# Kernel optimization log

Hardware: AMD Instinct MI355X
Metric: run time of the kernel (lower is better)

Reference implementation:

```python
import jax, jax.numpy as jnp
import numpy as np

NUM_KERNELS = 50
KERNEL_DIM = 5


def setup_inputs() -> dict:
    key = jax.random.key(0)
    k1, k2 = jax.random.split(key)
    B, F = 1024, 512
    x = jax.random.normal(k1, (B, F), dtype=jnp.float32)
    # glorot-uniform-ish scale for T
    fan_in, fan_out = F, NUM_KERNELS * KERNEL_DIM
    limit = float(np.sqrt(6.0 / (fan_in + fan_out)))
    T = jax.random.uniform(k2, (F, fan_out), dtype=jnp.float32, minval=-limit, maxval=limit)
    return {"x": x, "T": T}


def reference(x, T):
    B = x.shape[0]
    # M: [B, K, D]
    M = (x @ T).reshape(B, NUM_KERNELS, KERNEL_DIM)
    # pairwise diffs: [B, K, D, B]  (M[i,k,d] - M[j,k,d])
    diffs = M[:, :, :, None] - jnp.transpose(M, (1, 2, 0))[None, :, :, :]
    abs_diffs = jnp.sum(jnp.abs(diffs), axis=2)          # [B, K, B]
    minibatch_features = jnp.sum(jnp.exp(-abs_diffs), axis=2)  # [B, K]
    return jnp.concatenate([x, minibatch_features], axis=1)
```

## Files before the change

### kernel.cpp

```cpp
#include <hip/hip_runtime.h>

#define B_SZ 1024
#define F_SZ 512
#define NK   50
#define KD   5
#define C_SZ 250
#define OUTW 562
#define PLANE (C_SZ * B_SZ)
#define NT   16
#define TILE 64
#define NPAIRS 136
#define PART_ELEMS (NK * NT * B_SZ)
#define LOG2E 1.44269504088896340736f

__global__ __launch_bounds__(256) void gemm_copy_kernel(const float* __restrict__ x,
                                                        const float* __restrict__ T,
                                                        float* __restrict__ ws2,
                                                        float* __restrict__ out,
                                                        int zero_feat) {
    const int t = threadIdx.x;

    if (blockIdx.x >= 256) {
        const int b = blockIdx.x - 256;
#pragma unroll
        for (int r = 0; r < 8; ++r) {
            const int row = b * 8 + r;
            const float2* src = (const float2*)(x + (size_t)row * F_SZ);
            float2* dst = (float2*)(out + (size_t)row * OUTW);
            dst[t] = src[t];
            if (zero_feat && t < NK) out[(size_t)row * OUTW + F_SZ + t] = 0.0f;
        }
        return;
    }

    const int rt = blockIdx.x & 127;
    const int ks = blockIdx.x >> 7;
    if (t >= C_SZ) return;
    const int r0 = rt * 8;
    const int f0 = ks * 256;

    float acc[8] = {0.f, 0.f, 0.f, 0.f, 0.f, 0.f, 0.f, 0.f};
    const float* xp = x + (size_t)r0 * F_SZ + f0;
    const float* Tp = T + (size_t)f0 * C_SZ + t;

#pragma unroll 8
    for (int f = 0; f < 256; ++f) {
        const float tv = Tp[(size_t)f * C_SZ];
#pragma unroll
        for (int r = 0; r < 8; ++r)
            acc[r] += xp[r * F_SZ + f] * tv;
    }

    float* dst = ws2 + ((size_t)(ks * C_SZ + t)) * B_SZ + r0;
    float4 lo = make_float4(acc[0] * LOG2E, acc[1] * LOG2E,
                            acc[2] * LOG2E, acc[3] * LOG2E);
    float4 hi = make_float4(acc[4] * LOG2E, acc[5] * LOG2E,
                            acc[6] * LOG2E, acc[7] * LOG2E);
    ((float4*)dst)[0] = lo;
    ((float4*)dst)[1] = hi;
}

template <bool ATOMIC>
__global__ __launch_bounds__(256) void pair_kernel(const float* __restrict__ ws2,
                                                   float* __restrict__ part,
                                                   float* __restrict__ out) {
    const int bid = blockIdx.x;
    const int k = bid / NPAIRS;
    int p = bid - k * NPAIRS;
    int ti = 0;
    while (p >= NT - ti) { p -= NT - ti; ++ti; }
    const int tj = ti + p;

    const int t    = threadIdx.x;
    const int lane = t & 63;
    const int jq   = t >> 6;

    __shared__ __align__(16) float qi[KD][TILE];
    __shared__ __align__(16) float qj[KD][TILE];
    __shared__ float et[TILE][TILE + 1];
    __shared__ float rowp[4][TILE];
    __shared__ float colp[4][TILE];

    const float* pa = ws2 + (size_t)k * KD * B_SZ;
    const float* pb = pa + (size_t)PLANE;

    if (t < TILE) {
#pragma unroll
        for (int d = 0; d < KD; ++d) {
            const int row = ti * TILE + t;
            qi[d][t] = pa[d * B_SZ + row] + pb[d * B_SZ + row];
        }
    } else if (t < 2 * TILE) {
        const int l = t - TILE;
#pragma unroll
        for (int d = 0; d < KD; ++d) {
            const int row = tj * TILE + l;
            qj[d][l] = pa[d * B_SZ + row] + pb[d * B_SZ + row];
        }
    }
    __syncthreads();

    float m0 = qi[0][lane], m1 = qi[1][lane], m2 = qi[2][lane],
          m3 = qi[3][lane], m4 = qi[4][lane];
    float acc = 0.0f;
#pragma unroll
    for (int c4 = 0; c4 < 4; ++c4) {
        const int j0 = jq * 16 + c4 * 4;
        const float4 c0 = *(const float4*)&qj[0][j0];
        const float4 c1 = *(const float4*)&qj[1][j0];
        const float4 c2 = *(const float4*)&qj[2][j0];
        const float4 c3 = *(const float4*)&qj[3][j0];
        const float4 c4_ = *(const float4*)&qj[4][j0];
#define PAIR_ONE(C, JOFF)                                                        \
        {                                                                        \
            const float s = __builtin_fabsf(m0 - c0.C)                           \
                          + __builtin_fabsf(m1 - c1.C)                           \
                          + __builtin_fabsf(m2 - c2.C)                           \
                          + __builtin_fabsf(m3 - c3.C)                           \
                          + __builtin_fabsf(m4 - c4_.C);                         \
            const float e = __builtin_amdgcn_exp2f(-s);                          \
            acc += e;                                                            \
            et[j0 + JOFF][lane] = e;                                             \
        }
        PAIR_ONE(x, 0) PAIR_ONE(y, 1) PAIR_ONE(z, 2) PAIR_ONE(w, 3)
#undef PAIR_ONE
    }
    rowp[jq][lane] = acc;
    __syncthreads();

    if (ti != tj) {
        float csum = 0.0f;
#pragma unroll
        for (int e = 0; e < 16; ++e) csum += et[lane][jq * 16 + e];
        colp[jq][lane] = csum;
    }

    if (t < TILE) {
        const float r = rowp[0][t] + rowp[1][t] + rowp[2][t] + rowp[3][t];
        const int row = ti * TILE + t;
        if (ATOMIC) atomicAdd(&out[(size_t)row * OUTW + F_SZ + k], r);
        else        part[((size_t)(k * NT + tj)) * B_SZ + row] = r;
    }

    if (ti != tj) {
        __syncthreads();
        if (t < TILE) {
            const float c = colp[0][t] + colp[1][t] + colp[2][t] + colp[3][t];
            const int row = tj * TILE + t;
            if (ATOMIC) atomicAdd(&out[(size_t)row * OUTW + F_SZ + k], c);
            else        part[((size_t)(k * NT + ti)) * B_SZ + row] = c;
        }
    }
}

__global__ __launch_bounds__(256) void reduce_kernel(const float* __restrict__ part,
                                                     float* __restrict__ out) {
    const int k = blockIdx.x >> 2;
    const int i = ((blockIdx.x & 3) << 8) | threadIdx.x;
    float s = 0.0f;
#pragma unroll
    for (int sp = 0; sp < NT; ++sp)
        s += part[((size_t)(k * NT + sp)) * B_SZ + i];
    out[(size_t)i * OUTW + F_SZ + k] = s;
}

extern "C" void kernel_launch(void* const* d_in, const int* in_sizes, int n_in,
                              void* d_out, int out_size, void* d_ws, size_t ws_size,
                              hipStream_t stream) {
    const float* x = (const float*)d_in[0];
    const float* T = (const float*)d_in[1];
    float* out = (float*)d_out;
    float* ws2 = (float*)d_ws;
    float* part = ws2 + 2 * (size_t)PLANE;

    const size_t need = (size_t)(2 * PLANE + PART_ELEMS) * 4;
    const int fast = (ws_size >= need);

    gemm_copy_kernel<<<384, 256, 0, stream>>>(x, T, ws2, out, fast ? 0 : 1);

    if (fast) {
        pair_kernel<false><<<NK * NPAIRS, 256, 0, stream>>>(ws2, part, out);
        reduce_kernel<<<200, 256, 0, stream>>>(part, out);
    } else {
        pair_kernel<true><<<NK * NPAIRS, 256, 0, stream>>>(ws2, nullptr, out);
    }
}
```

Before: 35.70 us.

## Drop GEMM split-K and recompute symmetric pair tile instead of LDS transpose

```diff
diff --git a/kernel.cpp b/kernel.cpp
--- a/kernel.cpp
+++ b/kernel.cpp
@@ -15,13 +15,13 @@
 
 __global__ __launch_bounds__(256) void gemm_copy_kernel(const float* __restrict__ x,
                                                         const float* __restrict__ T,
-                                                        float* __restrict__ ws2,
+                                                        float* __restrict__ mp,
                                                         float* __restrict__ out,
                                                         int zero_feat) {
     const int t = threadIdx.x;
 
-    if (blockIdx.x >= 256) {
-        const int b = blockIdx.x - 256;
+    if (blockIdx.x >= 512) {
+        const int b = blockIdx.x - 512;
 #pragma unroll
         for (int r = 0; r < 8; ++r) {
             const int row = b * 8 + r;
@@ -33,35 +33,27 @@
         return;
     }
 
-    const int rt = blockIdx.x & 127;
-    const int ks = blockIdx.x >> 7;
+    const int rt = blockIdx.x;
     if (t >= C_SZ) return;
-    const int r0 = rt * 8;
-    const int f0 = ks * 256;
+    const int r0 = rt * 2;
 
-    float acc[8] = {0.f, 0.f, 0.f, 0.f, 0.f, 0.f, 0.f, 0.f};
-    const float* xp = x + (size_t)r0 * F_SZ + f0;
-    const float* Tp = T + (size_t)f0 * C_SZ + t;
+    float acc0 = 0.f, acc1 = 0.f;
+    const float* xp = x + (size_t)r0 * F_SZ;
+    const float* Tp = T + t;
 
-#pragma unroll 8
-    for (int f = 0; f < 256; ++f) {
+#pragma unroll 16
+    for (int f = 0; f < F_SZ; ++f) {
         const float tv = Tp[(size_t)f * C_SZ];
-#pragma unroll
-        for (int r = 0; r < 8; ++r)
-            acc[r] += xp[r * F_SZ + f] * tv;
+        acc0 += xp[f] * tv;
+        acc1 += xp[F_SZ + f] * tv;
     }
 
-    float* dst = ws2 + ((size_t)(ks * C_SZ + t)) * B_SZ + r0;
-    float4 lo = make_float4(acc[0] * LOG2E, acc[1] * LOG2E,
-                            acc[2] * LOG2E, acc[3] * LOG2E);
-    float4 hi = make_float4(acc[4] * LOG2E, acc[5] * LOG2E,
-                            acc[6] * LOG2E, acc[7] * LOG2E);
-    ((float4*)dst)[0] = lo;
-    ((float4*)dst)[1] = hi;
+    float2* dst = (float2*)(mp + (size_t)t * B_SZ + r0);
+    *dst = make_float2(acc0 * LOG2E, acc1 * LOG2E);
 }
 
 template <bool ATOMIC>
-__global__ __launch_bounds__(256) void pair_kernel(const float* __restrict__ ws2,
+__global__ __launch_bounds__(256) void pair_kernel(const float* __restrict__ mp,
                                                    float* __restrict__ part,
                                                    float* __restrict__ out) {
     const int bid = blockIdx.x;
@@ -73,83 +65,73 @@
 
     const int t    = threadIdx.x;
     const int lane = t & 63;
-    const int jq   = t >> 6;
+    const int jq   = __builtin_amdgcn_readfirstlane(threadIdx.x >> 6);
 
-    __shared__ __align__(16) float qi[KD][TILE];
-    __shared__ __align__(16) float qj[KD][TILE];
-    __shared__ float et[TILE][TILE + 1];
     __shared__ float rowp[4][TILE];
     __shared__ float colp[4][TILE];
 
-    const float* pa = ws2 + (size_t)k * KD * B_SZ;
-    const float* pb = pa + (size_t)PLANE;
+    const float* pk = mp + (size_t)k * (KD * B_SZ);
+    const int bi = ti * TILE;
+    const int bj = tj * TILE;
 
-    if (t < TILE) {
+    float mi[KD], mj[KD];
 #pragma unroll
-        for (int d = 0; d < KD; ++d) {
-            const int row = ti * TILE + t;
-            qi[d][t] = pa[d * B_SZ + row] + pb[d * B_SZ + row];
-        }
-    } else if (t < 2 * TILE) {
-        const int l = t - TILE;
-#pragma unroll
-        for (int d = 0; d < KD; ++d) {
-            const int row = tj * TILE + l;
-            qj[d][l] = pa[d * B_SZ + row] + pb[d * B_SZ + row];
-        }
+    for (int d = 0; d < KD; ++d) {
+        mi[d] = pk[d * B_SZ + bi + lane];
+        mj[d] = pk[d * B_SZ + bj + lane];
     }
-    __syncthreads();
 
-    float m0 = qi[0][lane], m1 = qi[1][lane], m2 = qi[2][lane],
-          m3 = qi[3][lane], m4 = qi[4][lane];
-    float acc = 0.0f;
+    const bool diag = (ti == tj);
+    float acci = 0.f, accj = 0.f;
+
+#define ESUM(mm, c0v, c1v, c2v, c3v, c4v, C)                                     \
+    __builtin_amdgcn_exp2f(-(__builtin_fabsf(mm[0] - c0v.C)                      \
+                           + __builtin_fabsf(mm[1] - c1v.C)                      \
+                           + __builtin_fabsf(mm[2] - c2v.C)                      \
+                           + __builtin_fabsf(mm[3] - c3v.C)                      \
+                           + __builtin_fabsf(mm[4] - c4v.C)))
+
 #pragma unroll
     for (int c4 = 0; c4 < 4; ++c4) {
         const int j0 = jq * 16 + c4 * 4;
-        const float4 c0 = *(const float4*)&qj[0][j0];
-        const float4 c1 = *(const float4*)&qj[1][j0];
-        const float4 c2 = *(const float4*)&qj[2][j0];
-        const float4 c3 = *(const float4*)&qj[3][j0];
-        const float4 c4_ = *(const float4*)&qj[4][j0];
-#define PAIR_ONE(C, JOFF)                                                        \
-        {                                                                        \
-            const float s = __builtin_fabsf(m0 - c0.C)                           \
-                          + __builtin_fabsf(m1 - c1.C)                           \
-                          + __builtin_fabsf(m2 - c2.C)                           \
-                          + __builtin_fabsf(m3 - c3.C)                           \
-                          + __builtin_fabsf(m4 - c4_.C);                         \
-            const float e = __builtin_amdgcn_exp2f(-s);                          \
-            acc += e;                                                            \
-            et[j0 + JOFF][lane] = e;                                             \
+
+        const float4 cj0 = *(const float4*)(pk + 0 * B_SZ + bj + j0);
+        const float4 cj1 = *(const float4*)(pk + 1 * B_SZ + bj + j0);
+        const float4 cj2 = *(const float4*)(pk + 2 * B_SZ + bj + j0);
+        const float4 cj3 = *(const float4*)(pk + 3 * B_SZ + bj + j0);
+        const float4 cj4 = *(const float4*)(pk + 4 * B_SZ + bj + j0);
+        acci += ESUM(mi, cj0, cj1, cj2, cj3, cj4, x);
+        acci += ESUM(mi, cj0, cj1, cj2, cj3, cj4, y);
+        acci += ESUM(mi, cj0, cj1, cj2, cj3, cj4, z);
+        acci += ESUM(mi, cj0, cj1, cj2, cj3, cj4, w);
+
+        if (!diag) {
+            const float4 ci0 = *(const float4*)(pk + 0 * B_SZ + bi + j0);
+            const float4 ci1 = *(const float4*)(pk + 1 * B_SZ + bi + j0);
+            const float4 ci2 = *(const float4*)(pk + 2 * B_SZ + bi + j0);
+            const float4 ci3 = *(const float4*)(pk + 3 * B_SZ + bi + j0);
+            const float4 ci4 = *(const float4*)(pk + 4 * B_SZ + bi + j0);
+            accj += ESUM(mj, ci0, ci1, ci2, ci3, ci4, x);
+            accj += ESUM(mj, ci0, ci1, ci2, ci3, ci4, y);
+            accj += ESUM(mj, ci0, ci1, ci2, ci3, ci4, z);
+            accj += ESUM(mj, ci0, ci1, ci2, ci3, ci4, w);
         }
-        PAIR_ONE(x, 0) PAIR_ONE(y, 1) PAIR_ONE(z, 2) PAIR_ONE(w, 3)
-#undef PAIR_ONE
     }
-    rowp[jq][lane] = acc;
+#undef ESUM
+
+    rowp[jq][lane] = acci;
+    if (!diag) colp[jq][lane] = accj;
     __syncthreads();
-
-    if (ti != tj) {
-        float csum = 0.0f;
-#pragma unroll
-        for (int e = 0; e < 16; ++e) csum += et[lane][jq * 16 + e];
-        colp[jq][lane] = csum;
-    }
 
     if (t < TILE) {
         const float r = rowp[0][t] + rowp[1][t] + rowp[2][t] + rowp[3][t];
-        const int row = ti * TILE + t;
-        if (ATOMIC) atomicAdd(&out[(size_t)row * OUTW + F_SZ + k], r);
-        else        part[((size_t)(k * NT + tj)) * B_SZ + row] = r;
-    }
-
-    if (ti != tj) {
-        __syncthreads();
-        if (t < TILE) {
-            const float c = colp[0][t] + colp[1][t] + colp[2][t] + colp[3][t];
-            const int row = tj * TILE + t;
-            if (ATOMIC) atomicAdd(&out[(size_t)row * OUTW + F_SZ + k], c);
-            else        part[((size_t)(k * NT + ti)) * B_SZ + row] = c;
-        }
+        if (ATOMIC) atomicAdd(&out[(size_t)(bi + t) * OUTW + F_SZ + k], r);
+        else        part[(size_t)(k * NT + tj) * B_SZ + bi + t] = r;
+    } else if (!diag && t < 2 * TILE) {
+        const int l = t - TILE;
+        const float c = colp[0][l] + colp[1][l] + colp[2][l] + colp[3][l];
+        if (ATOMIC) atomicAdd(&out[(size_t)(bj + l) * OUTW + F_SZ + k], c);
+        else        part[(size_t)(k * NT + ti) * B_SZ + bj + l] = c;
     }
 }
 
@@ -170,18 +152,18 @@
     const float* x = (const float*)d_in[0];
     const float* T = (const float*)d_in[1];
     float* out = (float*)d_out;
-    float* ws2 = (float*)d_ws;
-    float* part = ws2 + 2 * (size_t)PLANE;
+    float* mp  = (float*)d_ws;
+    float* part = mp + (size_t)PLANE;
 
-    const size_t need = (size_t)(2 * PLANE + PART_ELEMS) * 4;
+    const size_t need = (size_t)(PLANE + PART_ELEMS) * 4;
     const int fast = (ws_size >= need);
 
-    gemm_copy_kernel<<<384, 256, 0, stream>>>(x, T, ws2, out, fast ? 0 : 1);
+    gemm_copy_kernel<<<640, 256, 0, stream>>>(x, T, mp, out, fast ? 0 : 1);
 
     if (fast) {
-        pair_kernel<false><<<NK * NPAIRS, 256, 0, stream>>>(ws2, part, out);
+        pair_kernel<false><<<NK * NPAIRS, 256, 0, stream>>>(mp, part, out);
         reduce_kernel<<<200, 256, 0, stream>>>(part, out);
     } else {
-        pair_kernel<true><<<NK * NPAIRS, 256, 0, stream>>>(ws2, nullptr, out);
+        pair_kernel<true><<<NK * NPAIRS, 256, 0, stream>>>(mp, nullptr, out);
     }
 }
```

After: 40.73 us. 14.1% more time.

## Map one tile pair per wavefront using readlane broadcast and DPP column sums

Applied to the files above, without the earlier changes.

```diff
diff --git a/kernel.cpp b/kernel.cpp
--- a/kernel.cpp
+++ b/kernel.cpp
@@ -10,6 +10,7 @@
 #define NT   16
 #define TILE 64
 #define NPAIRS 136
+#define PBLK  34
 #define PART_ELEMS (NK * NT * B_SZ)
 #define LOG2E 1.44269504088896340736f
 
@@ -60,96 +61,84 @@
     ((float4*)dst)[1] = hi;
 }
 
+__device__ __forceinline__ float dpp_sum64(float v) {
+    int r = __float_as_int(v);
+    int t;
+    t = __builtin_amdgcn_update_dpp(0, r, 0x111, 0xf, 0xf, true);
+    r = __float_as_int(__int_as_float(r) + __int_as_float(t));
+    t = __builtin_amdgcn_update_dpp(0, r, 0x112, 0xf, 0xf, true);
+    r = __float_as_int(__int_as_float(r) + __int_as_float(t));
+    t = __builtin_amdgcn_update_dpp(0, r, 0x114, 0xf, 0xf, true);
+    r = __float_as_int(__int_as_float(r) + __int_as_float(t));
+    t = __builtin_amdgcn_update_dpp(0, r, 0x118, 0xf, 0xf, true);
+    r = __float_as_int(__int_as_float(r) + __int_as_float(t));
+    t = __builtin_amdgcn_update_dpp(0, r, 0x142, 0xa, 0xf, false);
+    r = __float_as_int(__int_as_float(r) + __int_as_float(t));
+    t = __builtin_amdgcn_update_dpp(0, r, 0x143, 0xc, 0xf, false);
+    r = __float_as_int(__int_as_float(r) + __int_as_float(t));
+    return __int_as_float(r);
+}
+
 template <bool ATOMIC>
-__global__ __launch_bounds__(256) void pair_kernel(const float* __restrict__ ws2,
+__global__ __launch_bounds__(256) void pair_kernel(const float* __restrict__ mp,
                                                    float* __restrict__ part,
                                                    float* __restrict__ out) {
     const int bid = blockIdx.x;
-    const int k = bid / NPAIRS;
-    int p = bid - k * NPAIRS;
+    const int k   = bid / PBLK;
+    const int wv  = __builtin_amdgcn_readfirstlane(threadIdx.x >> 6);
+    const int lane = threadIdx.x & 63;
+
+    int p = (bid - k * PBLK) * 4 + wv;
     int ti = 0;
     while (p >= NT - ti) { p -= NT - ti; ++ti; }
     const int tj = ti + p;
+    const int bi = ti * TILE;
+    const int bj = tj * TILE;
+    const bool diag = (ti == tj);
 
-    const int t    = threadIdx.x;
-    const int lane = t & 63;
-    const int jq   = t >> 6;
-
-    __shared__ __align__(16) float qi[KD][TILE];
-    __shared__ __align__(16) float qj[KD][TILE];
-    __shared__ float et[TILE][TILE + 1];
-    __shared__ float rowp[4][TILE];
-    __shared__ float colp[4][TILE];
-
-    const float* pa = ws2 + (size_t)k * KD * B_SZ;
+    const float* pa = mp + (size_t)k * (KD * B_SZ);
     const float* pb = pa + (size_t)PLANE;
 
-    if (t < TILE) {
+    float mi[KD], mj[KD];
 #pragma unroll
-        for (int d = 0; d < KD; ++d) {
-            const int row = ti * TILE + t;
-            qi[d][t] = pa[d * B_SZ + row] + pb[d * B_SZ + row];
-        }
-    } else if (t < 2 * TILE) {
-        const int l = t - TILE;
+    for (int d = 0; d < KD; ++d) {
+        mi[d] = pa[d * B_SZ + bi + lane] + pb[d * B_SZ + bi + lane];
+        mj[d] = pa[d * B_SZ + bj + lane] + pb[d * B_SZ + bj + lane];
+    }
+
+    float acci = 0.0f;
+    float vcol = 0.0f;
+
 #pragma unroll
-        for (int d = 0; d < KD; ++d) {
-            const int row = tj * TILE + l;
-            qj[d][l] = pa[d * B_SZ + row] + pb[d * B_SZ + row];
+    for (int j = 0; j < TILE; ++j) {
+        const float c0 = __int_as_float(__builtin_amdgcn_readlane(__float_as_int(mj[0]), j));
+        const float c1 = __int_as_float(__builtin_amdgcn_readlane(__float_as_int(mj[1]), j));
+        const float c2 = __int_as_float(__builtin_amdgcn_readlane(__float_as_int(mj[2]), j));
+        const float c3 = __int_as_float(__builtin_amdgcn_readlane(__float_as_int(mj[3]), j));
+        const float c4 = __int_as_float(__builtin_amdgcn_readlane(__float_as_int(mj[4]), j));
+        const float s = __builtin_fabsf(mi[0] - c0)
+                      + __builtin_fabsf(mi[1] - c1)
+                      + __builtin_fabsf(mi[2] - c2)
+                      + __builtin_fabsf(mi[3] - c3)
+                      + __builtin_fabsf(mi[4] - c4);
+        const float e = __builtin_amdgcn_exp2f(-s);
+        acci += e;
+        if (!diag) {
+            const float cs = dpp_sum64(e);
+            const float csf = __int_as_float(
+                __builtin_amdgcn_readlane(__float_as_int(cs), 63));
+            vcol = (lane == j) ? csf : vcol;
         }
     }
-    __syncthreads();
 
-    float m0 = qi[0][lane], m1 = qi[1][lane], m2 = qi[2][lane],
-          m3 = qi[3][lane], m4 = qi[4][lane];
-    float acc = 0.0f;
-#pragma unroll
-    for (int c4 = 0; c4 < 4; ++c4) {
-        const int j0 = jq * 16 + c4 * 4;
-        const float4 c0 = *(const float4*)&qj[0][j0];
-        const float4 c1 = *(const float4*)&qj[1][j0];
-        const float4 c2 = *(const float4*)&qj[2][j0];
-        const float4 c3 = *(const float4*)&qj[3][j0];
-        const float4 c4_ = *(const float4*)&qj[4][j0];
-#define PAIR_ONE(C, JOFF)                                                        \
-        {                                                                        \
-            const float s = __builtin_fabsf(m0 - c0.C)                           \
-                          + __builtin_fabsf(m1 - c1.C)                           \
-                          + __builtin_fabsf(m2 - c2.C)                           \
-                          + __builtin_fabsf(m3 - c3.C)                           \
-                          + __builtin_fabsf(m4 - c4_.C);                         \
-            const float e = __builtin_amdgcn_exp2f(-s);                          \
-            acc += e;                                                            \
-            et[j0 + JOFF][lane] = e;                                             \
-        }
-        PAIR_ONE(x, 0) PAIR_ONE(y, 1) PAIR_ONE(z, 2) PAIR_ONE(w, 3)
-#undef PAIR_ONE
-    }
-    rowp[jq][lane] = acc;
-    __syncthreads();
-
-    if (ti != tj) {
-        float csum = 0.0f;
-#pragma unroll
-        for (int e = 0; e < 16; ++e) csum += et[lane][jq * 16 + e];
-        colp[jq][lane] = csum;
-    }
-
-    if (t < TILE) {
-        const float r = rowp[0][t] + rowp[1][t] + rowp[2][t] + rowp[3][t];
-        const int row = ti * TILE + t;
-        if (ATOMIC) atomicAdd(&out[(size_t)row * OUTW + F_SZ + k], r);
-        else        part[((size_t)(k * NT + tj)) * B_SZ + row] = r;
-    }
-
-    if (ti != tj) {
-        __syncthreads();
-        if (t < TILE) {
-            const float c = colp[0][t] + colp[1][t] + colp[2][t] + colp[3][t];
-            const int row = tj * TILE + t;
-            if (ATOMIC) atomicAdd(&out[(size_t)row * OUTW + F_SZ + k], c);
-            else        part[((size_t)(k * NT + ti)) * B_SZ + row] = c;
-        }
+    if (ATOMIC) {
+        atomicAdd(&out[(size_t)(bi + lane) * OUTW + F_SZ + k], acci);
+        if (!diag)
+            atomicAdd(&out[(size_t)(bj + lane) * OUTW + F_SZ + k], vcol);
+    } else {
+        part[(size_t)(k * NT + tj) * B_SZ + bi + lane] = acci;
+        if (!diag)
+            part[(size_t)(k * NT + ti) * B_SZ + bj + lane] = vcol;
     }
 }
 
@@ -179,9 +168,9 @@
     gemm_copy_kernel<<<384, 256, 0, stream>>>(x, T, ws2, out, fast ? 0 : 1);
 
     if (fast) {
-        pair_kernel<false><<<NK * NPAIRS, 256, 0, stream>>>(ws2, part, out);
+        pair_kernel<false><<<NK * PBLK, 256, 0, stream>>>(ws2, part, out);
         reduce_kernel<<<200, 256, 0, stream>>>(part, out);
     } else {
-        pair_kernel<true><<<NK * NPAIRS, 256, 0, stream>>>(ws2, nullptr, out);
+        pair_kernel<true><<<NK * PBLK, 256, 0, stream>>>(ws2, nullptr, out);
     }
 }
```

New measurement: 47.20 us. +32.2%, slower.
